# Performance work log

Hardware: AMD Instinct MI355X
Metric: run time of the kernel (lower is better)

The kernel has to match this reference:

```python
import jax, jax.numpy as jnp
import numpy as np

B, S, D = 1, 4096, 512      # batch, seq, model dim
E, K, H = 64, 2, 256        # routed experts, top-k, expert hidden (moe_inter_dim)
HS = 2048                   # shared expert hidden = n_shared_experts * inter_dim
EPS = 1e-5                  # LayerNorm eps (torch default)


def setup_inputs() -> dict:
    key = jax.random.key(0)
    ks = jax.random.split(key, 16)
    n = lambda k, shp, s=0.02: jax.random.normal(k, shp, dtype=jnp.float32) * s
    return {
        "x": jax.random.normal(ks[0], (B, S, D), dtype=jnp.float32),
        # gate Linear(dim -> E)
        "Wg": n(ks[1], (E, D)), "bg": n(ks[2], (E,)),
        # per-expert LayerNorm affine
        "gamma": 1.0 + n(ks[3], (E, D)), "beta": n(ks[4], (E, D)),
        # per-expert SwiGLU: w1, w3: D->H ; w2: H->D
        "W1": n(ks[5], (E, D, H)), "b1": n(ks[6], (E, H)),
        "W3": n(ks[7], (E, D, H)), "b3": n(ks[8], (E, H)),
        "W2": n(ks[9], (E, H, D)), "b2": n(ks[10], (E, D)),
        # shared expert (same Expert structure, hidden HS)
        "gs": 1.0 + n(ks[11], (D,)), "bs": n(ks[11], (D,)),
        "Ws1": n(ks[12], (D, HS)), "bs1": n(ks[12], (HS,)),
        "Ws3": n(ks[13], (D, HS)), "bs3": n(ks[13], (HS,)),
        "Ws2": n(ks[14], (HS, D)), "bs2": n(ks[15], (D,)),
    }


def reference(x, Wg, bg, gamma, beta, W1, b1, W3, b3, W2, b2,
              gs, bs, Ws1, bs1, Ws3, bs3, Ws2, bs2):
    shape = x.shape
    xt = x.reshape(-1, D)                      # [T, D] tokens
    T = xt.shape[0]

    # ---- Gate (eval path: sigmoid scores, no load balancing / bias / groups) ----
    scores = jax.nn.sigmoid(xt @ Wg.T + bg)    # [T, E]
    w, idx = jax.lax.top_k(scores, K)          # [T, K]
    w = w / w.sum(-1, keepdims=True)           # sigmoid path normalization; route_scale = 1
    # dense combine weights: cw[t, e] = routing weight of token t on expert e (0 if not routed)
    cw = jnp.zeros((T, E), xt.dtype).at[jnp.arange(T)[:, None], idx].add(w)

    # ---- Shared LayerNorm statistics (affine folded per-expert below) ----
    mu = xt.mean(-1, keepdims=True)
    var = ((xt - mu) ** 2).mean(-1, keepdims=True)
    nx = (xt - mu) * jax.lax.rsqrt(var + EPS)  # [T, D], unit-affine normalized

    # Fold each expert's LN affine (gamma_e, beta_e) into its w1/w3:
    # (nx*g + b) @ W = nx @ (g[:,None]*W) + b @ W
    W1p = gamma[:, :, None] * W1
    b1p = b1 + jnp.einsum('ed,edh->eh', beta, W1)
    W3p = gamma[:, :, None] * W3
    b3p = b3 + jnp.einsum('ed,edh->eh', beta, W3)

    h1 = jnp.einsum('td,edh->eth', nx, W1p) + b1p[:, None, :]   # [E, T, H]
    h3 = jnp.einsum('td,edh->eth', nx, W3p) + b3p[:, None, :]
    h = jax.nn.silu(h1) * h3                                     # SwiGLU, [E, T, H]

    # Weighted combine: y[t] = sum_e cw[t,e] * (h[e,t] @ W2[e] + b2[e])
    hw = h * cw.T[:, :, None]                                    # [E, T, H]
    y = jnp.einsum('eth,ehd->td', hw, W2) + cw @ b2              # [T, D]

    # ---- Shared expert (applied to every token) ----
    nxs = nx * gs + bs
    hs = jax.nn.silu(nxs @ Ws1 + bs1) * (nxs @ Ws3 + bs3)        # [T, HS]
    z = hs @ Ws2 + bs2

    return (y + z).reshape(shape)
```

## Files before the change

kernel.cpp:

```cpp
#include <hip/hip_runtime.h>
#include <math.h>

typedef unsigned short u16;
typedef unsigned int u32;
typedef __attribute__((ext_vector_type(8))) short bf16x8;
typedef __attribute__((ext_vector_type(4))) float f32x4;

#define TT   4096
#define DM   512
#define NE   64
#define HE   256
#define HSH  2048
#define NSH  8
#define PADBASE 16384
#define MAXTILES 384
#define MAXRT    128

#define WAITV(N) asm volatile("s_waitcnt vmcnt(" #N ")" ::: "memory")
#define SBAR()   __builtin_amdgcn_s_barrier()
#define SCHEDB() __builtin_amdgcn_sched_barrier(0)

__device__ __forceinline__ float sig_(float z){ return 1.f/(1.f+__expf(-z)); }

__device__ __forceinline__ u16 f2bf(float x){
  u32 u = __builtin_bit_cast(u32, x);
  u = (u + 0x7FFFu + ((u >> 16) & 1u)) >> 16;
  return (u16)u;
}

__device__ __forceinline__ f32x4 mfma16(bf16x8 a, bf16x8 b, f32x4 c){
  return __builtin_amdgcn_mfma_f32_16x16x32_bf16(a, b, c, 0, 0, 0);
}

__device__ __forceinline__ bf16x8 frd(const char* tile, int row, int csw){
  return *(const bf16x8*)(tile + row*64 + csw);
}

__device__ __forceinline__ void gl16(const void* g, void* l){
  __builtin_amdgcn_global_load_lds(
      (const __attribute__((address_space(1))) unsigned int*)g,
      (__attribute__((address_space(3))) unsigned int*)l, 16, 0, 0);
}

struct CvtJob {
  const float* in; const float* scale; const float* fvec;
  u16* out; float* fout; int K; int N; int base;
};
struct CvtJobs { CvtJob j[6]; };

__global__ __launch_bounds__(256) void k_pre(
    CvtJobs jobs, int ln_base,
    const float* __restrict__ x, const float* __restrict__ Wg,
    const float* __restrict__ bg,
    u16* __restrict__ nxb, int* __restrict__ top_idx, float* __restrict__ top_w)
{
  __shared__ __align__(16) char LT[256*144];
  const int bid = blockIdx.x;
  const int tid = threadIdx.x;

  if (bid < ln_base){
    int ji = 0;
    #pragma unroll
    for (int i = 1; i < 6; i++) ji = (bid >= jobs.j[i].base) ? i : ji;
    const CvtJob J = jobs.j[ji];
    const int local = bid - J.base;
    const int nbk = J.K >> 6;
    const int nbn = J.N >> 8;
    const int pm = nbk * nbn;
    const int z = local / pm, rem = local - z*pm;
    const int kt = rem % nbk, ntile = rem / nbk;
    const int k0 = kt*64;
    const int n  = ntile*256 + tid;

    const float* src = J.in + (size_t)z*J.K*J.N + (size_t)k0*J.N + n;
    const float* scp = J.scale ? (J.scale + (size_t)z*J.K + k0) : nullptr;
    const float* fvp = J.fvec  ? (J.fvec  + (size_t)z*J.K + k0) : nullptr;

    float fsum = 0.f;
    #pragma unroll 2
    for (int kk = 0; kk < 8; kk++){
      float v[8];
      #pragma unroll
      for (int j = 0; j < 8; j++) v[j] = src[(size_t)(kk*8 + j)*J.N];
      u16 b[8];
      if (scp){
        #pragma unroll
        for (int j = 0; j < 8; j++) b[j] = f2bf(v[j]*scp[kk*8 + j]);
      } else {
        #pragma unroll
        for (int j = 0; j < 8; j++) b[j] = f2bf(v[j]);
      }
      if (fvp){
        #pragma unroll
        for (int j = 0; j < 8; j++) fsum += v[j]*fvp[kk*8 + j];
      }
      uint4 pk;
      pk.x = (u32)b[0] | ((u32)b[1] << 16);
      pk.y = (u32)b[2] | ((u32)b[3] << 16);
      pk.z = (u32)b[4] | ((u32)b[5] << 16);
      pk.w = (u32)b[6] | ((u32)b[7] << 16);
      *(uint4*)(LT + tid*144 + kk*16) = pk;
    }
    if (J.fout) atomicAdd(J.fout + (size_t)z*J.N + n, fsum);
    __syncthreads();

    u16* obase = J.out + (size_t)z*J.K*J.N + (size_t)(ntile*256)*J.K + k0;
    #pragma unroll 2
    for (int cc = 0; cc < 8; cc++){
      const int g = cc*256 + tid;
      const int row = g >> 3, ch = g & 7;
      uint4 v = *(const uint4*)(LT + row*144 + ch*16);
      *(uint4*)(obase + (size_t)row*J.K + ch*8) = v;
    }
    return;
  }

  __shared__ float xs[DM];
  __shared__ float sred[4], ssred[4];
  __shared__ float sc[NE];
  const int t = bid - ln_base;

  float2 v = reinterpret_cast<const float2*>(x + (size_t)t*DM)[tid];
  xs[2*tid]   = v.x;
  xs[2*tid+1] = v.y;
  float s  = v.x + v.y;
  float ss = v.x*v.x + v.y*v.y;
  #pragma unroll
  for (int o = 32; o > 0; o >>= 1){ s += __shfl_xor(s, o); ss += __shfl_xor(ss, o); }
  const int wid = tid >> 6, lane = tid & 63;
  if (lane == 0){ sred[wid] = s; ssred[wid] = ss; }
  __syncthreads();
  const float tot = sred[0]+sred[1]+sred[2]+sred[3];
  const float tss = ssred[0]+ssred[1]+ssred[2]+ssred[3];
  const float mu  = tot * (1.f/DM);
  const float var = tss * (1.f/DM) - mu*mu;
  const float rstd = rsqrtf(var + 1e-5f);
  u32 pk = (u32)f2bf((v.x-mu)*rstd) | ((u32)f2bf((v.y-mu)*rstd) << 16);
  *(u32*)(nxb + (size_t)t*DM + 2*tid) = pk;

  const int e = tid >> 2, sub = tid & 3;
  const float4* wrow4 = reinterpret_cast<const float4*>(Wg + (size_t)e*DM);
  const float4* xs4   = reinterpret_cast<const float4*>(xs);
  float acc = 0.f;
  #pragma unroll 4
  for (int i = sub; i < DM/4; i += 4){
    const float4 w = wrow4[i]; const float4 xv = xs4[i];
    acc += xv.x*w.x + xv.y*w.y + xv.z*w.z + xv.w*w.w;
  }
  acc += __shfl_xor(acc, 1);
  acc += __shfl_xor(acc, 2);
  if (sub == 0) sc[e] = acc + bg[e];
  __syncthreads();

  if (tid < 64) {
    const float s0 = sc[tid];
    float m = s0; int mi = tid;
    #pragma unroll
    for (int o = 1; o < 64; o <<= 1){
      float om = __shfl_xor(m, o); int oi = __shfl_xor(mi, o);
      if (om > m || (om == m && oi < mi)) { m = om; mi = oi; }
    }
    float s1 = (tid == mi) ? -INFINITY : s0;
    float m2 = s1; int mi2 = tid;
    #pragma unroll
    for (int o = 1; o < 64; o <<= 1){
      float om = __shfl_xor(m2, o); int oi = __shfl_xor(mi2, o);
      if (om > m2 || (om == m2 && oi < mi2)) { m2 = om; mi2 = oi; }
    }
    if (tid == 0){
      const float w0 = sig_(m), w1 = sig_(m2);
      const float inv = 1.f/(w0+w1);
      top_idx[2*t]   = mi;
      top_idx[2*t+1] = mi2;
      top_w[2*t]     = w0*inv;
      top_w[2*t+1]   = w1*inv;
    }
  }
}

__global__ __launch_bounds__(256) void k_route(
    const int* __restrict__ top_idx, const float* __restrict__ top_w,
    int* __restrict__ bucket_tok, float* __restrict__ bucket_w,
    int* __restrict__ tiles, int* __restrict__ n_tiles)
{
  __shared__ int cnt[NE], base_[NE];
  __shared__ int nroute;
  const int tid = threadIdx.x;
  if (tid < NE) cnt[tid] = 0;
  __syncthreads();
  for (int p = tid; p < TT*2; p += 256) atomicAdd(&cnt[top_idx[p]], 1);
  __syncthreads();
  if (tid == 0){
    int run = 0, ntl = 0;
    for (int e = 0; e < NE; e++){
      base_[e] = run;
      const int c = cnt[e];
      for (int b = 0; b < c; b += 128){
        const int n = (c - b < 128) ? (c - b) : 128;
        tiles[ntl++] = (e << 17) | (((run + b) >> 7) << 8) | n;
      }
      run += ((c + 127) >> 7) << 7;
    }
    nroute = ntl;
    n_tiles[0] = ntl + NSH*(TT/128);
    n_tiles[1] = ntl;
  }
  __syncthreads();
  if (tid < NSH*(TT/128)){
    const int s = tid >> 5, t = tid & 31;
    const int b0 = PADBASE + s*TT + t*128;
    tiles[nroute + tid] = ((NE + s) << 17) | ((b0 >> 7) << 8) | 128;
  }
  if (tid < NE) cnt[tid] = 0;
  __syncthreads();
  for (int p = tid; p < TT*2; p += 256){
    const int e = top_idx[p];
    const int pos = base_[e] + atomicAdd(&cnt[e], 1);
    bucket_tok[pos] = p >> 1;
    bucket_w[pos]   = top_w[p];
  }
}

__global__ __launch_bounds__(512) void k_up(
    const u16* __restrict__ nxb,
    const u16* __restrict__ W1bT, const u16* __restrict__ W3bT,
    const u16* __restrict__ Ws1bT, const u16* __restrict__ Ws3bT,
    const float* __restrict__ b1, const float* __restrict__ b3,
    const float* __restrict__ bs1, const float* __restrict__ bs3,
    const float* __restrict__ b1f, const float* __restrict__ b3f,
    const int* __restrict__ bucket_tok, const float* __restrict__ bucket_w,
    const int* __restrict__ tiles, const int* __restrict__ n_tiles,
    u16* __restrict__ hrout, u16* __restrict__ hs)
{
  if ((int)blockIdx.x >= n_tiles[0]) return;
  const int info = tiles[blockIdx.x];
  const int e  = info >> 17;
  const int b0 = ((info >> 8) & 0x1FF) << 7;
  const int nt = info & 255;
  const bool sh = (e >= NE);
  const int y  = blockIdx.y;

  __shared__ __align__(16) char Ab[3][8192];
  __shared__ __align__(16) char B1b[3][8192];
  __shared__ __align__(16) char B3b[3][8192];
  __shared__ int   toks[128];
  __shared__ float tw[128];

  const int tid = threadIdx.x, wid = tid >> 6, lane = tid & 63;
  const int l15 = lane & 15, q = lane >> 4;

  if (tid < 128){
    int tk; float w;
    if (!sh){
      if (tid < nt){ tk = bucket_tok[b0+tid]; w = bucket_w[b0+tid]; }
      else         { tk = 0; w = 0.f; }
    } else {
      tk = ((b0 - PADBASE) & (TT-1)) + tid; w = 1.f;
    }
    toks[tid] = tk; tw[tid] = w;
  }
  __syncthreads();

  const u16* w1e = sh ? (Ws1bT + (size_t)(e-NE)*HE*DM) : (W1bT + (size_t)e*HE*DM);
  const u16* w3e = sh ? (Ws3bT + (size_t)(e-NE)*HE*DM) : (W3bT + (size_t)e*HE*DM);

  const int srow = lane >> 2;
  const int csrc = (((lane & 3) ^ ((lane >> 3) & 3))) * 8;
  const u16* asrc = nxb + (size_t)toks[wid*16 + srow]*DM + csrc;
  const u16* b1s  = w1e + (size_t)(y*128 + wid*16 + srow)*DM + csrc;
  const u16* b3s  = w3e + (size_t)(y*128 + wid*16 + srow)*DM + csrc;
  const int loff = wid*1024;

#define UP_STAGE(ph, k0) do{ \
    gl16(asrc + (k0), Ab[ph] + loff); \
    gl16(b1s  + (k0), B1b[ph] + loff); \
    gl16(b3s  + (k0), B3b[ph] + loff); \
  } while(0)

  const int wm = (wid & 1)*64, wn = (wid >> 1)*32;

  const float* ob1 = sh ? (bs1 + (size_t)(e-NE)*HE) : (b1 + (size_t)e*HE);
  const float* ob3 = sh ? (bs3 + (size_t)(e-NE)*HE) : (b3 + (size_t)e*HE);
  f32x4 acc1[4][2], acc3[4][2];
  #pragma unroll
  for (int fn = 0; fn < 2; fn++){
    const int h = y*128 + wn + fn*16 + l15;
    const float v1 = ob1[h] + b1f[(size_t)e*HE + h];
    const float v3 = ob3[h] + b3f[(size_t)e*HE + h];
    #pragma unroll
    for (int fm = 0; fm < 4; fm++){
      acc1[fm][fn] = (f32x4){v1,v1,v1,v1};
      acc3[fm][fn] = (f32x4){v3,v3,v3,v3};
    }
  }

  UP_STAGE(0, 0);
  UP_STAGE(1, 32);
  const int csw = (q ^ ((l15 >> 1) & 3)) * 16;

  for (int ks = 0; ks < DM/32; ks++){
    const int cur = ks % 3;
    if (ks + 2 < DM/32) UP_STAGE((ks+2)%3, (ks+2)*32);
    if (ks < DM/32 - 2)       WAITV(6);
    else if (ks == DM/32 - 2) WAITV(3);
    else                      WAITV(0);
    SBAR();
    __builtin_amdgcn_s_setprio(1);
    const char* A  = Ab[cur];
    const char* B1 = B1b[cur];
    const char* B3 = B3b[cur];
    bf16x8 fa[4];
    #pragma unroll
    for (int fm = 0; fm < 4; fm++) fa[fm] = frd(A, wm + fm*16 + l15, csw);
    #pragma unroll
    for (int fn = 0; fn < 2; fn++){
      bf16x8 fb1 = frd(B1, wn + fn*16 + l15, csw);
      bf16x8 fb3 = frd(B3, wn + fn*16 + l15, csw);
      #pragma unroll
      for (int fm = 0; fm < 4; fm++){
        acc1[fm][fn] = mfma16(fa[fm], fb1, acc1[fm][fn]);
        acc3[fm][fn] = mfma16(fa[fm], fb3, acc3[fm][fn]);
      }
    }
    __builtin_amdgcn_s_setprio(0);
    SCHEDB();
    SBAR();
  }
#undef UP_STAGE

  const int tbase = sh ? ((b0 - PADBASE) & (TT-1)) : 0;
  const int scol  = sh ? (e - NE)*HE : 0;
  #pragma unroll
  for (int fm = 0; fm < 4; fm++){
    #pragma unroll
    for (int fn = 0; fn < 2; fn++){
      const int hl = y*128 + wn + fn*16 + l15;
      #pragma unroll
      for (int r = 0; r < 4; r++){
        const int m = wm + fm*16 + 4*q + r;
        float v = 0.f;
        if (m < nt){
          const float a1 = acc1[fm][fn][r];
          const float a3 = acc3[fm][fn][r];
          v = a1 * sig_(a1) * a3 * tw[m];
        }
        if (sh) hs[(size_t)(tbase+m)*HSH + scol + hl] = f2bf(v);
        else    hrout[(size_t)(b0+m)*HE + hl] = f2bf(v);
      }
    }
  }
}

__global__ __launch_bounds__(512) void k_down(
    const u16* __restrict__ hs, const u16* __restrict__ Ws2bT,
    const float* __restrict__ bs2,
    const u16* __restrict__ hrout, const u16* __restrict__ W2bT,
    const float* __restrict__ b2,
    const int* __restrict__ bucket_tok, const float* __restrict__ bucket_w,
    const int* __restrict__ tiles, const int* __restrict__ n_tiles,
    float* __restrict__ out)
{
  __shared__ __align__(16) char LDS[73728];
  __shared__ int   toks[128];
  __shared__ float tw[128];

  const int tid = threadIdx.x, wid = tid >> 6, lane = tid & 63;
  const int l15 = lane & 15, q = lane >> 4;
  const int csw  = (q ^ ((l15 >> 1) & 3)) * 16;
  const int srow = tid >> 2;
  const int csrc = ((tid & 3) ^ ((tid >> 3) & 3)) * 8;
  const int loff = wid*1024;

  if ((int)blockIdx.x < 128){
    const int t0 = (blockIdx.x >> 2) * 128;
    const int d0 = (blockIdx.x & 3) * 128;
    char* Ab = LDS;
    char* Bb = LDS + 24576;

    const u16* asrc = hs    + (size_t)(t0 + srow)*HSH + csrc;
    const u16* bsrc = Ws2bT + (size_t)(d0 + srow)*HSH + csrc;

#define DS_STAGE(ph, k0) do{ \
    gl16(asrc + (k0), Ab + (ph)*8192 + loff); \
    gl16(bsrc + (k0), Bb + (ph)*8192 + loff); \
  } while(0)

    const int wm = (wid & 1)*64, wn = (wid >> 1)*32;

    f32x4 acc[4][2];
    #pragma unroll
    for (int fm = 0; fm < 4; fm++)
      #pragma unroll
      for (int fn = 0; fn < 2; fn++) acc[fm][fn] = (f32x4){0.f,0.f,0.f,0.f};

    DS_STAGE(0, 0);
    DS_STAGE(1, 32);

    for (int ks = 0; ks < HSH/32; ks++){
      const int cur = ks % 3;
      if (ks + 2 < HSH/32) DS_STAGE((ks+2)%3, (ks+2)*32);
      if (ks < HSH/32 - 2)       WAITV(4);
      else if (ks == HSH/32 - 2) WAITV(2);
      else                       WAITV(0);
      SBAR();
      __builtin_amdgcn_s_setprio(1);
      const char* A = Ab + cur*8192;
      const char* B = Bb + cur*8192;
      bf16x8 fa[4];
      #pragma unroll
      for (int fm = 0; fm < 4; fm++) fa[fm] = frd(A, wm + fm*16 + l15, csw);
      #pragma unroll
      for (int fn = 0; fn < 2; fn++){
        bf16x8 fb = frd(B, wn + fn*16 + l15, csw);
        #pragma unroll
        for (int fm = 0; fm < 4; fm++)
          acc[fm][fn] = mfma16(fa[fm], fb, acc[fm][fn]);
      }
      __builtin_amdgcn_s_setprio(0);
      SCHEDB();
      SBAR();
    }
#undef DS_STAGE

    #pragma unroll
    for (int fm = 0; fm < 4; fm++){
      #pragma unroll
      for (int fn = 0; fn < 2; fn++){
        const int d = d0 + wn + fn*16 + l15;
        const float bv = bs2[d];
        #pragma unroll
        for (int r = 0; r < 4; r++){
          const int t = t0 + wm + fm*16 + 4*q + r;
          atomicAdd(out + (size_t)t*DM + d, acc[fm][fn][r] + bv);
        }
      }
    }
    return;
  }

  const int rb = (int)blockIdx.x - 128;
  const int ti = rb >> 1;
  if (ti >= n_tiles[1]) return;
  const int info = tiles[ti];
  const int e  = info >> 17;
  const int b0 = ((info >> 8) & 0x1FF) << 7;
  const int nt = info & 255;
  const int d0 = (rb & 1) * 256;

  char* Ab = LDS;
  char* Bb = LDS + 24576;

  if (tid < 128){
    if (tid < nt){ toks[tid] = bucket_tok[b0+tid]; tw[tid] = bucket_w[b0+tid]; }
    else         { toks[tid] = 0; tw[tid] = 0.f; }
  }
  __syncthreads();

  const u16* w2e = W2bT + (size_t)e*DM*HE;
  const u16* asrc  = hrout + (size_t)(b0 + srow)*HE + csrc;
  const u16* bsrc0 = w2e + (size_t)(d0 + srow)*HE + csrc;
  const u16* bsrc1 = w2e + (size_t)(d0 + 128 + srow)*HE + csrc;

#define DR_STAGE(ph, k0) do{ \
    gl16(asrc  + (k0), Ab + (ph)*8192  + loff); \
    gl16(bsrc0 + (k0), Bb + (ph)*16384 + loff); \
    gl16(bsrc1 + (k0), Bb + (ph)*16384 + 8192 + loff); \
  } while(0)

  const int wm = (wid & 1)*64, wn = (wid >> 1)*64;

  f32x4 acc[4][4];
  #pragma unroll
  for (int fm = 0; fm < 4; fm++)
    #pragma unroll
    for (int fn = 0; fn < 4; fn++) acc[fm][fn] = (f32x4){0.f,0.f,0.f,0.f};

  DR_STAGE(0, 0);
  DR_STAGE(1, 32);

  for (int ks = 0; ks < HE/32; ks++){
    const int cur = ks % 3;
    if (ks + 2 < HE/32) DR_STAGE((ks+2)%3, (ks+2)*32);
    if (ks < HE/32 - 2)       WAITV(6);
    else if (ks == HE/32 - 2) WAITV(3);
    else                      WAITV(0);
    SBAR();
    __builtin_amdgcn_s_setprio(1);
    const char* A = Ab + cur*8192;
    const char* B = Bb + cur*16384;
    bf16x8 fa[4];
    #pragma unroll
    for (int fm = 0; fm < 4; fm++) fa[fm] = frd(A, wm + fm*16 + l15, csw);
    #pragma unroll
    for (int fn = 0; fn < 4; fn++){
      bf16x8 fb = frd(B, wn + fn*16 + l15, csw);
      #pragma unroll
      for (int fm = 0; fm < 4; fm++)
        acc[fm][fn] = mfma16(fa[fm], fb, acc[fm][fn]);
    }
    __builtin_amdgcn_s_setprio(0);
    SCHEDB();
    SBAR();
  }
#undef DR_STAGE

  #pragma unroll
  for (int fm = 0; fm < 4; fm++){
    #pragma unroll
    for (int fn = 0; fn < 4; fn++){
      const int d = d0 + wn + fn*16 + l15;
      #pragma unroll
      for (int r = 0; r < 4; r++){
        const int m = wm + fm*16 + 4*q + r;
        if (m < nt)
          atomicAdd(out + (size_t)toks[m]*DM + d, acc[fm][fn][r] + tw[m]*b2[(size_t)e*DM + d]);
      }
    }
  }
}

extern "C" void kernel_launch(void* const* d_in, const int* in_sizes, int n_in,
                              void* d_out, int out_size, void* d_ws, size_t ws_size,
                              hipStream_t stream)
{
  (void)in_sizes; (void)n_in; (void)ws_size;
  const float* x     = (const float*)d_in[0];
  const float* Wg    = (const float*)d_in[1];
  const float* bg    = (const float*)d_in[2];
  const float* gamma = (const float*)d_in[3];
  const float* beta  = (const float*)d_in[4];
  const float* W1    = (const float*)d_in[5];
  const float* b1    = (const float*)d_in[6];
  const float* W3    = (const float*)d_in[7];
  const float* b3    = (const float*)d_in[8];
  const float* W2    = (const float*)d_in[9];
  const float* b2    = (const float*)d_in[10];
  const float* gs    = (const float*)d_in[11];
  const float* bs    = (const float*)d_in[12];
  const float* Ws1   = (const float*)d_in[13];
  const float* bs1   = (const float*)d_in[14];
  const float* Ws3   = (const float*)d_in[15];
  const float* bs3   = (const float*)d_in[16];
  const float* Ws2   = (const float*)d_in[17];
  const float* bs2   = (const float*)d_in[18];
  float* out = (float*)d_out;

  char* ws = (char*)d_ws;
  size_t off = 0;
  auto alloc = [&](size_t bytes) -> char* {
    char* p = ws + off;
    off += (bytes + 255) & ~(size_t)255;
    return p;
  };
  u16*   nxb        = (u16*)  alloc((size_t)TT*DM*2);
  int*   top_idx    = (int*)  alloc((size_t)TT*2*4);
  float* top_w      = (float*)alloc((size_t)TT*2*4);
  int*   bucket_tok = (int*)  alloc((size_t)PADBASE*4);
  float* bucket_w   = (float*)alloc((size_t)PADBASE*4);
  int*   tiles      = (int*)  alloc(MAXTILES*4);
  int*   n_tiles    = (int*)  alloc(64);
  u16*   hrout      = (u16*)  alloc((size_t)PADBASE*HE*2);
  u16*   hs         = (u16*)  alloc((size_t)TT*HSH*2);
  u16*   W1bT       = (u16*)  alloc((size_t)NE*HE*DM*2);
  u16*   W3bT       = (u16*)  alloc((size_t)NE*HE*DM*2);
  u16*   W2bT       = (u16*)  alloc((size_t)NE*DM*HE*2);
  u16*   Ws1bT      = (u16*)  alloc((size_t)HSH*DM*2);
  u16*   Ws3bT      = (u16*)  alloc((size_t)HSH*DM*2);
  u16*   Ws2bT      = (u16*)  alloc((size_t)DM*HSH*2);
  float* b1f        = (float*)alloc((size_t)(NE*HE + HSH)*4);
  float* b3f        = (float*)alloc((size_t)(NE*HE + HSH)*4);

  hipMemsetAsync(b1f, 0, (size_t)(NE*HE + HSH)*4, stream);
  hipMemsetAsync(b3f, 0, (size_t)(NE*HE + HSH)*4, stream);
  hipMemsetAsync(out, 0, (size_t)out_size*sizeof(float), stream);

  CvtJobs jobs;
  jobs.j[0] = { W1,  gamma,   beta,    W1bT,  b1f,          DM,  HE,  0    };
  jobs.j[1] = { W3,  gamma,   beta,    W3bT,  b3f,          DM,  HE,  512  };
  jobs.j[2] = { W2,  nullptr, nullptr, W2bT,  nullptr,      HE,  DM,  1024 };
  jobs.j[3] = { Ws1, gs,      bs,      Ws1bT, b1f + NE*HE,  DM,  HSH, 1536 };
  jobs.j[4] = { Ws3, gs,      bs,      Ws3bT, b3f + NE*HE,  DM,  HSH, 1600 };
  jobs.j[5] = { Ws2, nullptr, nullptr, Ws2bT, nullptr,      HSH, DM,  1664 };
  const int ln_base = 1728;
  k_pre<<<dim3(ln_base + TT), 256, 0, stream>>>(jobs, ln_base,
                                                x, Wg, bg, nxb, top_idx, top_w);

  k_route<<<dim3(1), 256, 0, stream>>>(top_idx, top_w, bucket_tok, bucket_w, tiles, n_tiles);

  k_up<<<dim3(MAXTILES, 2), 512, 0, stream>>>(nxb, W1bT, W3bT, Ws1bT, Ws3bT,
                                              b1, b3, bs1, bs3, b1f, b3f,
                                              bucket_tok, bucket_w, tiles, n_tiles, hrout, hs);
  k_down<<<dim3(384), 512, 0, stream>>>(hs, Ws2bT, bs2, hrout, W2bT, b2,
                                        bucket_tok, bucket_w, tiles, n_tiles, out);
}
```

Baseline: 198.1 us.

## Template weight conversion, double-buffer GEMM stages, split-K shared down projection

Weight conversion in k_pre now uses compile-time K/N template instantiations instead of a runtime job table, which removes the job lookup and runtime index division, and its load loop unroll goes from 2 to 4. The up and down GEMM kernels drop from triple to double buffering, shrinking LDS per block to allow more resident blocks, at the cost of less prefetch depth. The shared-expert down projection is split four ways along K (512 blocks instead of 128) and accumulates into output atomically, with the bias added only by the first K-chunk. This raises parallelism and occupancy but adds more atomic traffic and shortens the prefetch pipeline.

```diff
diff --git a/kernel.cpp b/kernel.cpp
--- a/kernel.cpp
+++ b/kernel.cpp
@@ -42,14 +42,71 @@
       (__attribute__((address_space(3))) unsigned int*)l, 16, 0, 0);
 }
 
-struct CvtJob {
-  const float* in; const float* scale; const float* fvec;
-  u16* out; float* fout; int K; int N; int base;
-};
-struct CvtJobs { CvtJob j[6]; };
+template<int K, int N>
+__device__ __forceinline__ void cvt_tile(
+    const float* __restrict__ in, const float* __restrict__ scale,
+    const float* __restrict__ fvec, u16* __restrict__ out,
+    float* __restrict__ fout, int local, int tid, char* LT)
+{
+  const int nbk = K >> 6;
+  const int nbn = N >> 8;
+  const int pm = nbk * nbn;
+  const int z = local / pm, rem = local - z*pm;
+  const int kt = rem % nbk, ntile = rem / nbk;
+  const int k0 = kt*64;
+  const int n  = ntile*256 + tid;
+
+  const float* src = in + (size_t)z*K*N + (size_t)k0*N + n;
+  const float* scp = scale ? (scale + (size_t)z*K + k0) : nullptr;
+  const float* fvp = fvec  ? (fvec  + (size_t)z*K + k0) : nullptr;
+
+  float fsum = 0.f;
+  #pragma unroll 4
+  for (int kk = 0; kk < 8; kk++){
+    float v[8];
+    #pragma unroll
+    for (int j = 0; j < 8; j++) v[j] = src[(size_t)(kk*8 + j)*N];
+    u16 b[8];
+    if (scp){
+      #pragma unroll
+      for (int j = 0; j < 8; j++) b[j] = f2bf(v[j]*scp[kk*8 + j]);
+    } else {
+      #pragma unroll
+      for (int j = 0; j < 8; j++) b[j] = f2bf(v[j]);
+    }
+    if (fvp){
+      #pragma unroll
+      for (int j = 0; j < 8; j++) fsum += v[j]*fvp[kk*8 + j];
+    }
+    uint4 pk;
+    pk.x = (u32)b[0] | ((u32)b[1] << 16);
+    pk.y = (u32)b[2] | ((u32)b[3] << 16);
+    pk.z = (u32)b[4] | ((u32)b[5] << 16);
+    pk.w = (u32)b[6] | ((u32)b[7] << 16);
+    *(uint4*)(LT + tid*144 + kk*16) = pk;
+  }
+  if (fout) atomicAdd(fout + (size_t)z*N + n, fsum);
+  __syncthreads();
+
+  u16* obase = out + (size_t)z*K*N + (size_t)(ntile*256)*K + k0;
+  #pragma unroll 2
+  for (int cc = 0; cc < 8; cc++){
+    const int g = cc*256 + tid;
+    const int row = g >> 3, ch = g & 7;
+    uint4 v = *(const uint4*)(LT + row*144 + ch*16);
+    *(uint4*)(obase + (size_t)row*K + ch*8) = v;
+  }
+}
 
 __global__ __launch_bounds__(256) void k_pre(
-    CvtJobs jobs, int ln_base,
+    const float* __restrict__ W1, const float* __restrict__ W3,
+    const float* __restrict__ W2, const float* __restrict__ Ws1,
+    const float* __restrict__ Ws3, const float* __restrict__ Ws2,
+    const float* __restrict__ gamma, const float* __restrict__ beta,
+    const float* __restrict__ gs, const float* __restrict__ bsv,
+    u16* __restrict__ W1bT, u16* __restrict__ W3bT, u16* __restrict__ W2bT,
+    u16* __restrict__ Ws1bT, u16* __restrict__ Ws3bT, u16* __restrict__ Ws2bT,
+    float* __restrict__ b1f, float* __restrict__ b3f,
     const float* __restrict__ x, const float* __restrict__ Wg,
     const float* __restrict__ bg,
     u16* __restrict__ nxb, int* __restrict__ top_idx, float* __restrict__ top_w)
@@ -58,67 +115,20 @@
   const int bid = blockIdx.x;
   const int tid = threadIdx.x;
 
-  if (bid < ln_base){
-    int ji = 0;
-    #pragma unroll
-    for (int i = 1; i < 6; i++) ji = (bid >= jobs.j[i].base) ? i : ji;
-    const CvtJob J = jobs.j[ji];
-    const int local = bid - J.base;
-    const int nbk = J.K >> 6;
-    const int nbn = J.N >> 8;
-    const int pm = nbk * nbn;
-    const int z = local / pm, rem = local - z*pm;
-    const int kt = rem % nbk, ntile = rem / nbk;
-    const int k0 = kt*64;
-    const int n  = ntile*256 + tid;
-
-    const float* src = J.in + (size_t)z*J.K*J.N + (size_t)k0*J.N + n;
-    const float* scp = J.scale ? (J.scale + (size_t)z*J.K + k0) : nullptr;
-    const float* fvp = J.fvec  ? (J.fvec  + (size_t)z*J.K + k0) : nullptr;
-
-    float fsum = 0.f;
-    #pragma unroll 2
-    for (int kk = 0; kk < 8; kk++){
-      float v[8];
-      #pragma unroll
-      for (int j = 0; j < 8; j++) v[j] = src[(size_t)(kk*8 + j)*J.N];
-      u16 b[8];
-      if (scp){
-        #pragma unroll
-        for (int j = 0; j < 8; j++) b[j] = f2bf(v[j]*scp[kk*8 + j]);
-      } else {
-        #pragma unroll
-        for (int j = 0; j < 8; j++) b[j] = f2bf(v[j]);
-      }
-      if (fvp){
-        #pragma unroll
-        for (int j = 0; j < 8; j++) fsum += v[j]*fvp[kk*8 + j];
-      }
-      uint4 pk;
-      pk.x = (u32)b[0] | ((u32)b[1] << 16);
-      pk.y = (u32)b[2] | ((u32)b[3] << 16);
-      pk.z = (u32)b[4] | ((u32)b[5] << 16);
-      pk.w = (u32)b[6] | ((u32)b[7] << 16);
-      *(uint4*)(LT + tid*144 + kk*16) = pk;
-    }
-    if (J.fout) atomicAdd(J.fout + (size_t)z*J.N + n, fsum);
-    __syncthreads();
-
-    u16* obase = J.out + (size_t)z*J.K*J.N + (size_t)(ntile*256)*J.K + k0;
-    #pragma unroll 2
-    for (int cc = 0; cc < 8; cc++){
-      const int g = cc*256 + tid;
-      const int row = g >> 3, ch = g & 7;
-      uint4 v = *(const uint4*)(LT + row*144 + ch*16);
-      *(uint4*)(obase + (size_t)row*J.K + ch*8) = v;
-    }
+  if (bid < 1728){
+    if      (bid < 512)  cvt_tile<DM,HE> (W1,  gamma,   beta,    W1bT,  b1f,        bid,      tid, LT);
+    else if (bid < 1024) cvt_tile<DM,HE> (W3,  gamma,   beta,    W3bT,  b3f,        bid-512,  tid, LT);
+    else if (bid < 1536) cvt_tile<HE,DM> (W2,  nullptr, nullptr, W2bT,  nullptr,    bid-1024, tid, LT);
+    else if (bid < 1600) cvt_tile<DM,HSH>(Ws1, gs,      bsv,     Ws1bT, b1f+NE*HE,  bid-1536, tid, LT);
+    else if (bid < 1664) cvt_tile<DM,HSH>(Ws3, gs,      bsv,     Ws3bT, b3f+NE*HE,  bid-1600, tid, LT);
+    else                 cvt_tile<HSH,DM>(Ws2, nullptr, nullptr, Ws2bT, nullptr,    bid-1664, tid, LT);
     return;
   }
 
   __shared__ float xs[DM];
   __shared__ float sred[4], ssred[4];
   __shared__ float sc[NE];
-  const int t = bid - ln_base;
+  const int t = bid - 1728;
 
   float2 v = reinterpret_cast<const float2*>(x + (size_t)t*DM)[tid];
   xs[2*tid]   = v.x;
@@ -240,9 +250,9 @@
   const bool sh = (e >= NE);
   const int y  = blockIdx.y;
 
-  __shared__ __align__(16) char Ab[3][8192];
-  __shared__ __align__(16) char B1b[3][8192];
-  __shared__ __align__(16) char B3b[3][8192];
+  __shared__ __align__(16) char Ab[2][8192];
+  __shared__ __align__(16) char B1b[2][8192];
+  __shared__ __align__(16) char B3b[2][8192];
   __shared__ int   toks[128];
   __shared__ float tw[128];
 
@@ -295,15 +305,12 @@
   }
 
   UP_STAGE(0, 0);
-  UP_STAGE(1, 32);
   const int csw = (q ^ ((l15 >> 1) & 3)) * 16;
 
   for (int ks = 0; ks < DM/32; ks++){
-    const int cur = ks % 3;
-    if (ks + 2 < DM/32) UP_STAGE((ks+2)%3, (ks+2)*32);
-    if (ks < DM/32 - 2)       WAITV(6);
-    else if (ks == DM/32 - 2) WAITV(3);
-    else                      WAITV(0);
+    const int cur = ks & 1;
+    if (ks + 1 < DM/32){ UP_STAGE(cur^1, (ks+1)*32); WAITV(3); }
+    else               { WAITV(0); }
     SBAR();
     __builtin_amdgcn_s_setprio(1);
     const char* A  = Ab[cur];
@@ -360,7 +367,7 @@
     const int* __restrict__ tiles, const int* __restrict__ n_tiles,
     float* __restrict__ out)
 {
-  __shared__ __align__(16) char LDS[73728];
+  __shared__ __align__(16) char LDS[49152];
   __shared__ int   toks[128];
   __shared__ float tw[128];
 
@@ -371,14 +378,15 @@
   const int csrc = ((tid & 3) ^ ((tid >> 3) & 3)) * 8;
   const int loff = wid*1024;
 
-  if ((int)blockIdx.x < 128){
-    const int t0 = (blockIdx.x >> 2) * 128;
-    const int d0 = (blockIdx.x & 3) * 128;
+  if ((int)blockIdx.x < 512){
+    const int kc = blockIdx.x & 3;
+    const int d0 = ((blockIdx.x >> 2) & 3) * 128;
+    const int t0 = (blockIdx.x >> 4) * 128;
     char* Ab = LDS;
-    char* Bb = LDS + 24576;
-
-    const u16* asrc = hs    + (size_t)(t0 + srow)*HSH + csrc;
-    const u16* bsrc = Ws2bT + (size_t)(d0 + srow)*HSH + csrc;
+    char* Bb = LDS + 16384;
+
+    const u16* asrc = hs    + (size_t)(t0 + srow)*HSH + kc*512 + csrc;
+    const u16* bsrc = Ws2bT + (size_t)(d0 + srow)*HSH + kc*512 + csrc;
 
 #define DS_STAGE(ph, k0) do{ \
     gl16(asrc + (k0), Ab + (ph)*8192 + loff); \
@@ -394,14 +402,11 @@
       for (int fn = 0; fn < 2; fn++) acc[fm][fn] = (f32x4){0.f,0.f,0.f,0.f};
 
     DS_STAGE(0, 0);
-    DS_STAGE(1, 32);
-
-    for (int ks = 0; ks < HSH/32; ks++){
-      const int cur = ks % 3;
-      if (ks + 2 < HSH/32) DS_STAGE((ks+2)%3, (ks+2)*32);
-      if (ks < HSH/32 - 2)       WAITV(4);
-      else if (ks == HSH/32 - 2) WAITV(2);
-      else                       WAITV(0);
+
+    for (int ks = 0; ks < 16; ks++){
+      const int cur = ks & 1;
+      if (ks + 1 < 16){ DS_STAGE(cur^1, (ks+1)*32); WAITV(2); }
+      else            { WAITV(0); }
       SBAR();
       __builtin_amdgcn_s_setprio(1);
       const char* A = Ab + cur*8192;
@@ -427,7 +432,7 @@
       #pragma unroll
       for (int fn = 0; fn < 2; fn++){
         const int d = d0 + wn + fn*16 + l15;
-        const float bv = bs2[d];
+        const float bv = (kc == 0) ? bs2[d] : 0.f;
         #pragma unroll
         for (int r = 0; r < 4; r++){
           const int t = t0 + wm + fm*16 + 4*q + r;
@@ -438,7 +443,7 @@
     return;
   }
 
-  const int rb = (int)blockIdx.x - 128;
+  const int rb = (int)blockIdx.x - 512;
   const int ti = rb >> 1;
   if (ti >= n_tiles[1]) return;
   const int info = tiles[ti];
@@ -448,7 +453,7 @@
   const int d0 = (rb & 1) * 256;
 
   char* Ab = LDS;
-  char* Bb = LDS + 24576;
+  char* Bb = LDS + 16384;
 
   if (tid < 128){
     if (tid < nt){ toks[tid] = bucket_tok[b0+tid]; tw[tid] = bucket_w[b0+tid]; }
@@ -476,14 +481,11 @@
     for (int fn = 0; fn < 4; fn++) acc[fm][fn] = (f32x4){0.f,0.f,0.f,0.f};
 
   DR_STAGE(0, 0);
-  DR_STAGE(1, 32);
 
   for (int ks = 0; ks < HE/32; ks++){
-    const int cur = ks % 3;
-    if (ks + 2 < HE/32) DR_STAGE((ks+2)%3, (ks+2)*32);
-    if (ks < HE/32 - 2)       WAITV(6);
-    else if (ks == HE/32 - 2) WAITV(3);
-    else                      WAITV(0);
+    const int cur = ks & 1;
+    if (ks + 1 < HE/32){ DR_STAGE(cur^1, (ks+1)*32); WAITV(3); }
+    else               { WAITV(0); }
     SBAR();
     __builtin_amdgcn_s_setprio(1);
     const char* A = Ab + cur*8192;
@@ -574,22 +576,16 @@
   hipMemsetAsync(b3f, 0, (size_t)(NE*HE + HSH)*4, stream);
   hipMemsetAsync(out, 0, (size_t)out_size*sizeof(float), stream);
 
-  CvtJobs jobs;
-  jobs.j[0] = { W1,  gamma,   beta,    W1bT,  b1f,          DM,  HE,  0    };
-  jobs.j[1] = { W3,  gamma,   beta,    W3bT,  b3f,          DM,  HE,  512  };
-  jobs.j[2] = { W2,  nullptr, nullptr, W2bT,  nullptr,      HE,  DM,  1024 };
-  jobs.j[3] = { Ws1, gs,      bs,      Ws1bT, b1f + NE*HE,  DM,  HSH, 1536 };
-  jobs.j[4] = { Ws3, gs,      bs,      Ws3bT, b3f + NE*HE,  DM,  HSH, 1600 };
-  jobs.j[5] = { Ws2, nullptr, nullptr, Ws2bT, nullptr,      HSH, DM,  1664 };
-  const int ln_base = 1728;
-  k_pre<<<dim3(ln_base + TT), 256, 0, stream>>>(jobs, ln_base,
-                                                x, Wg, bg, nxb, top_idx, top_w);
+  k_pre<<<dim3(1728 + TT), 256, 0, stream>>>(
+      W1, W3, W2, Ws1, Ws3, Ws2, gamma, beta, gs, bs,
+      W1bT, W3bT, W2bT, Ws1bT, Ws3bT, Ws2bT, b1f, b3f,
+      x, Wg, bg, nxb, top_idx, top_w);
 
   k_route<<<dim3(1), 256, 0, stream>>>(top_idx, top_w, bucket_tok, bucket_w, tiles, n_tiles);
 
   k_up<<<dim3(MAXTILES, 2), 512, 0, stream>>>(nxb, W1bT, W3bT, Ws1bT, Ws3bT,
                                               b1, b3, bs1, bs3, b1f, b3f,
                                               bucket_tok, bucket_w, tiles, n_tiles, hrout, hs);
-  k_down<<<dim3(384), 512, 0, stream>>>(hs, Ws2bT, bs2, hrout, W2bT, b2,
+  k_down<<<dim3(768), 512, 0, stream>>>(hs, Ws2bT, bs2, hrout, W2bT, b2,
                                         bucket_tok, bucket_w, tiles, n_tiles, out);
 }
```

Result: slower. 202.0 us (+2.0%).
